# Optimization experiments

Hardware: AMD Instinct MI355X
Metric: run time of the kernel (lower is better)

The kernel has to match this reference:

```python
import jax, jax.numpy as jnp
import numpy as np

KERNEL = 8


def setup_inputs() -> dict:
    key = jax.random.key(0)
    ks = jax.random.split(key, 9)
    N, Cin, L = 16, 128, 2048
    Cout = 256
    x = jax.random.normal(ks[0], (N, Cin, L), dtype=jnp.float32)
    conv_w = jax.random.normal(ks[1], (Cout, Cin, KERNEL), dtype=jnp.float32) * (1.0 / np.sqrt(Cin * KERNEL))
    conv_b = jax.random.normal(ks[2], (Cout,), dtype=jnp.float32) * 0.01
    wq = jax.random.normal(ks[3], (Cout, Cout), dtype=jnp.float32) * (1.0 / np.sqrt(Cout))
    bq = jax.random.normal(ks[4], (Cout,), dtype=jnp.float32) * 0.01
    wk = jax.random.normal(ks[5], (Cout, Cout), dtype=jnp.float32) * (1.0 / np.sqrt(Cout))
    bk = jax.random.normal(ks[6], (Cout,), dtype=jnp.float32) * 0.01
    wv = jax.random.normal(ks[7], (Cout, Cout), dtype=jnp.float32) * (1.0 / np.sqrt(Cout))
    bv = jax.random.normal(ks[8], (Cout,), dtype=jnp.float32) * 0.01
    return {"x": x, "conv_w": conv_w, "conv_b": conv_b,
            "wq": wq, "bq": bq, "wk": wk, "bk": bk, "wv": wv, "bv": bv}


def reference(x, conv_w, conv_b, wq, bq, wk, bk, wv, bv):
    # Conv1d, valid padding: [N, Cin, L] -> [N, Cout, S], S = L - KERNEL + 1
    h = jax.lax.conv_general_dilated(
        x, conv_w, window_strides=(1,), padding='VALID',
        dimension_numbers=('NCH', 'OIH', 'NCH'))
    h = jax.nn.relu(h + conv_b[None, :, None])
    N, C, S = h.shape
    h = jnp.transpose(h, (0, 2, 1))  # [N, S, C]
    # Linear layers (torch convention: y = x @ W^T + b)
    q = jnp.einsum('nsc,dc->nsd', h, wq) + bq
    k = jnp.einsum('nsc,dc->nsd', h, wk) + bk
    v = jnp.einsum('nsc,dc->nsd', h, wv) + bv
    # sigmoid (non-normalized) attention over full SxS scores
    scores = jnp.einsum('nsd,ntd->nst', q, k) / jnp.sqrt(jnp.asarray(C, h.dtype))
    attn = jax.nn.sigmoid(scores)  # [N, S, S]
    out = jnp.einsum('nst,ntd->nsd', attn, v)
    return jnp.transpose(out, (0, 2, 1))  # [N, C, S]
```

## Files before the change

kernel.cpp:

```cpp
#include <hip/hip_runtime.h>

typedef short short8 __attribute__((ext_vector_type(8)));
typedef float f32x4 __attribute__((ext_vector_type(4)));
typedef float f32x16 __attribute__((ext_vector_type(16)));
typedef unsigned short u16x4 __attribute__((ext_vector_type(4)));

constexpr int NB = 16, CIN = 128, LIN = 2048, CO = 256;
constexpr int SL = 2041;
constexpr int MT = NB * SL;
constexpr int MP = 32768;
constexpr int XTS = 136;

constexpr size_t XT_OFF = 0;
constexpr size_t XT_SZ  = (size_t)NB*LIN*XTS*2 + 65536;
constexpr size_t CW_OFF = XT_OFF + XT_SZ;
constexpr size_t CW_SZ  = (size_t)CO*CIN*8*2;
constexpr size_t WQ_OFF = CW_OFF + CW_SZ;
constexpr size_t WB_SZ  = (size_t)CO*CO*2;
constexpr size_t WK_OFF = WQ_OFF + WB_SZ;
constexpr size_t WV_OFF = WK_OFF + WB_SZ;
constexpr size_t H_OFF  = WV_OFF + WB_SZ;
constexpr size_t HB_SZ  = (size_t)MP*CO*2;
constexpr size_t Q_OFF  = H_OFF + HB_SZ;
constexpr size_t K_OFF  = Q_OFF + HB_SZ;
constexpr size_t VT_OFF = K_OFF + HB_SZ;

__device__ inline unsigned short f2bf(float f) {
  union { float f; unsigned int u; } v; v.f = f;
  unsigned int r = v.u + 0x7fffu + ((v.u >> 16) & 1u);
  return (unsigned short)(r >> 16);
}

__device__ inline void sync_lds() {
  __asm__ volatile("" ::: "memory");
  __builtin_amdgcn_s_waitcnt(0xc07f);
  __builtin_amdgcn_s_barrier();
  __asm__ volatile("" ::: "memory");
}
__device__ inline void barrier_only() {
  __asm__ volatile("" ::: "memory");
  __builtin_amdgcn_s_barrier();
  __asm__ volatile("" ::: "memory");
}

#if defined(__has_builtin)
#if __has_builtin(__builtin_amdgcn_global_load_lds)
#define HAVE_GLDS 1
#endif
#endif

__device__ inline void gld16(const unsigned short* g, void* l) {
#ifdef HAVE_GLDS
  __builtin_amdgcn_global_load_lds(
      (const __attribute__((address_space(1))) void*)g,
      (__attribute__((address_space(3))) void*)l, 16, 0, 0);
#else
  *(short8*)l = *(const short8*)g;
#endif
}

__device__ inline unsigned int cvt_pk_bf16(float a, float b) {
  unsigned int r;
  asm("v_cvt_pk_bf16_f32 %0, %1, %2" : "=v"(r) : "v"(a), "v"(b));
  return r;
}
__device__ inline void swap32(unsigned int& a, unsigned int& b) {
  asm("v_permlane32_swap_b32 %0, %1" : "+v"(a), "+v"(b));
}

__global__ void xpose_kernel(const float* __restrict__ x, unsigned short* __restrict__ xt) {
  __shared__ float tile[32][33];
  const int tx = threadIdx.x, ty = threadIdx.y;
  const int s0 = blockIdx.x * 32, c0 = blockIdx.y * 32, n = blockIdx.z;
  #pragma unroll
  for (int r = 0; r < 4; ++r)
    tile[ty * 4 + r][tx] = x[((size_t)(n * CIN + c0 + ty * 4 + r)) * LIN + s0 + tx];
  __syncthreads();
  #pragma unroll
  for (int r = 0; r < 4; ++r)
    xt[((size_t)(n * LIN + s0 + ty * 4 + r)) * XTS + c0 + tx] = f2bf(tile[tx][ty * 4 + r]);
}

__global__ void wconv_kernel(const float* __restrict__ w, unsigned short* __restrict__ o) {
  int idx = blockIdx.x * 256 + threadIdx.x;
  int co = idx >> 10, r = idx & 1023, kp = r >> 7, ci = r & 127;
  o[idx] = f2bf(w[co * 1024 + ci * 8 + kp]);
}

__global__ void wqkv_kernel(const float* __restrict__ a, const float* __restrict__ b,
                            const float* __restrict__ c, unsigned short* __restrict__ oa,
                            unsigned short* __restrict__ ob, unsigned short* __restrict__ oc) {
  int z = blockIdx.x >> 6, lb = blockIdx.x & 63;
  const float* src = (z == 0) ? a : (z == 1) ? b : c;
  unsigned short* dst = (z == 0) ? oa : (z == 1) ? ob : oc;
  int i = (lb * 256 + threadIdx.x) * 4;
  float4 v = *(const float4*)(src + i);
  u16x4 r;
  r.x = f2bf(v.x); r.y = f2bf(v.y); r.z = f2bf(v.z); r.w = f2bf(v.w);
  *(u16x4*)(dst + i) = r;
}

__global__ __launch_bounds__(256) void conv_gemm(
    const unsigned short* __restrict__ xt,
    const unsigned short* __restrict__ wb,
    const float* __restrict__ bias,
    unsigned short* __restrict__ h)
{
  __shared__ unsigned short sX[18432];
  __shared__ unsigned short sB[2][4096];
  const int tid = threadIdx.x;
  const int w = tid >> 6, lane = tid & 63, quad = lane >> 4, l16 = lane & 15;
  const int n  = blockIdx.y;
  const int s0 = blockIdx.x * 128;
  const int d0 = blockIdx.z * 128;

  {
    const unsigned short* xbase = xt + ((size_t)n * LIN + s0) * XTS;
    #pragma unroll
    for (int i = 0; i < 9; ++i) {
      int u = i * 256 + tid;
      gld16(xbase + u * 8, ((char*)sX) + u * 16);
    }
  }

  const int brow0 = tid >> 2, bkgs = tid & 3;
  short8 breg[2];
  #pragma unroll
  for (int i2 = 0; i2 < 2; ++i2) {
    int row = i2 * 64 + brow0;
    int kg = bkgs ^ ((row >> 1) & 3);
    breg[i2] = *(const short8*)(wb + (size_t)(d0 + row) * 1024 + kg * 8);
  }
  #pragma unroll
  for (int i2 = 0; i2 < 2; ++i2)
    *(short8*)(&sB[0][(i2 * 256 + tid) * 8]) = breg[i2];
  __syncthreads();

  f32x4 acc[2][8];
  #pragma unroll
  for (int i = 0; i < 2; ++i)
    #pragma unroll
    for (int j = 0; j < 8; ++j) acc[i][j] = (f32x4){0.f, 0.f, 0.f, 0.f};

  for (int kc = 0; kc < 32; ++kc) {
    const int kcn = (kc < 31) ? kc + 1 : kc;
    const int kpn = kcn >> 2, ci0n = (kcn & 3) * 32;
    #pragma unroll
    for (int i2 = 0; i2 < 2; ++i2) {
      int row = i2 * 64 + brow0;
      int kg = bkgs ^ ((row >> 1) & 3);
      breg[i2] = *(const short8*)(wb + (size_t)(d0 + row) * 1024 + kpn * 128 + ci0n + kg * 8);
    }

    const int kp = kc >> 2, ci0 = (kc & 3) * 32;
    const unsigned short* sBc = sB[kc & 1];
    short8 bfr[8];
    #pragma unroll
    for (int j = 0; j < 8; ++j) {
      int r = j * 16 + l16;
      bfr[j] = *(const short8*)(sBc + r * 32 + (quad ^ ((r >> 1) & 3)) * 8);
    }
    #pragma unroll
    for (int i = 0; i < 2; ++i) {
      int srow = w * 32 + i * 16 + l16;
      short8 afr = *(const short8*)(sX + (srow + kp) * XTS + ci0 + quad * 8);
      #pragma unroll
      for (int j = 0; j < 8; ++j)
        acc[i][j] = __builtin_amdgcn_mfma_f32_16x16x32_bf16(afr, bfr[j], acc[i][j], 0, 0, 0);
    }

    #pragma unroll
    for (int i2 = 0; i2 < 2; ++i2)
      *(short8*)(&sB[(kc + 1) & 1][(i2 * 256 + tid) * 8]) = breg[i2];
    sync_lds();
  }

  #pragma unroll
  for (int i = 0; i < 2; ++i)
    #pragma unroll
    for (int j = 0; j < 8; ++j) {
      int col = d0 + j * 16 + l16;
      float bv = bias[col];
      #pragma unroll
      for (int jj = 0; jj < 4; ++jj) {
        int s = s0 + w * 32 + i * 16 + quad * 4 + jj;
        if (s < SL) {
          float val = fmaxf(acc[i][j][jj] + bv, 0.f);
          h[(size_t)(n * SL + s) * CO + col] = f2bf(val);
        }
      }
    }
}

__global__ __launch_bounds__(256) void lin_gemm(
    const unsigned short* __restrict__ A,
    const unsigned short* __restrict__ Bq, const unsigned short* __restrict__ Bk,
    const unsigned short* __restrict__ Bv,
    const float* __restrict__ biq, const float* __restrict__ bik,
    const float* __restrict__ biv,
    unsigned short* __restrict__ qb, unsigned short* __restrict__ kb,
    unsigned short* __restrict__ vtb)
{
  __shared__ unsigned short sA[2][4096];
  __shared__ unsigned short sB[2][4096];
  const int tid = threadIdx.x;
  const int w = tid >> 6, lane = tid & 63, quad = lane >> 4, l16 = lane & 15;
  const int m0 = blockIdx.x * 128, d0 = blockIdx.y * 128, z = blockIdx.z;
  const unsigned short* B = (z == 0) ? Bq : (z == 1) ? Bk : Bv;
  const float* bias        = (z == 0) ? biq : (z == 1) ? bik : biv;

  const int brow0 = tid >> 2, bkgs = tid & 3;
  short8 areg[2], breg[2];
  #pragma unroll
  for (int i2 = 0; i2 < 2; ++i2) {
    int row = i2 * 64 + brow0;
    int kg = bkgs ^ ((row >> 1) & 3);
    areg[i2] = *(const short8*)(A + (size_t)(m0 + row) * CO + kg * 8);
    breg[i2] = *(const short8*)(B + (size_t)(d0 + row) * CO + kg * 8);
  }
  #pragma unroll
  for (int i2 = 0; i2 < 2; ++i2) {
    *(short8*)(&sA[0][(i2 * 256 + tid) * 8]) = areg[i2];
    *(short8*)(&sB[0][(i2 * 256 + tid) * 8]) = breg[i2];
  }
  sync_lds();

  f32x4 acc[2][8];
  #pragma unroll
  for (int i = 0; i < 2; ++i)
    #pragma unroll
    for (int j = 0; j < 8; ++j) acc[i][j] = (f32x4){0.f, 0.f, 0.f, 0.f};

  for (int kc = 0; kc < 8; ++kc) {
    const int kcn = (kc < 7) ? kc + 1 : kc;
    #pragma unroll
    for (int i2 = 0; i2 < 2; ++i2) {
      int row = i2 * 64 + brow0;
      int kg = bkgs ^ ((row >> 1) & 3);
      areg[i2] = *(const short8*)(A + (size_t)(m0 + row) * CO + kcn * 32 + kg * 8);
      breg[i2] = *(const short8*)(B + (size_t)(d0 + row) * CO + kcn * 32 + kg * 8);
    }

    const unsigned short* sAc = sA[kc & 1];
    const unsigned short* sBc = sB[kc & 1];
    short8 afr[2], bfr[8];
    #pragma unroll
    for (int i = 0; i < 2; ++i) {
      int r = w * 32 + i * 16 + l16;
      afr[i] = *(const short8*)(sAc + r * 32 + (quad ^ ((r >> 1) & 3)) * 8);
    }
    #pragma unroll
    for (int j = 0; j < 8; ++j) {
      int r = j * 16 + l16;
      bfr[j] = *(const short8*)(sBc + r * 32 + (quad ^ ((r >> 1) & 3)) * 8);
    }
    #pragma unroll
    for (int i = 0; i < 2; ++i)
      #pragma unroll
      for (int j = 0; j < 8; ++j)
        acc[i][j] = __builtin_amdgcn_mfma_f32_16x16x32_bf16(afr[i], bfr[j], acc[i][j], 0, 0, 0);

    #pragma unroll
    for (int i2 = 0; i2 < 2; ++i2) {
      *(short8*)(&sA[(kc + 1) & 1][(i2 * 256 + tid) * 8]) = areg[i2];
      *(short8*)(&sB[(kc + 1) & 1][(i2 * 256 + tid) * 8]) = breg[i2];
    }
    sync_lds();
  }

  #pragma unroll
  for (int i = 0; i < 2; ++i)
    #pragma unroll
    for (int j = 0; j < 8; ++j) {
      int col = d0 + j * 16 + l16;
      float bv = bias[col];
      #pragma unroll
      for (int jj = 0; jj < 4; ++jj) {
        int m = m0 + w * 32 + i * 16 + quad * 4 + jj;
        float val = acc[i][j][jj] + bv;
        if (z == 0) {
          qb[(size_t)m * CO + col] = f2bf(val * 0.0625f);
        } else if (z == 1) {
          kb[(size_t)m * CO + col] = f2bf(val);
        } else if (m < MT) {
          int nn = m / SL, ss = m - nn * SL;
          vtb[(size_t)col * MP + nn * 2048 + ss] = f2bf(val);
        }
      }
    }
}

__global__ __launch_bounds__(512, 2) void attn_kernel(
    const unsigned short* __restrict__ qb,
    const unsigned short* __restrict__ kb,
    const unsigned short* __restrict__ vtb,
    float* __restrict__ out)
{
  __shared__ unsigned short sK[2][16384];
  __shared__ unsigned short sV[2][16384];
  const int tid = threadIdx.x;
  const int w = tid >> 6, lane = tid & 63;
  const int half = lane >> 5, l32 = lane & 31;
  const int bidx = blockIdx.x;
  const int n = (bidx & 7) + ((bidx >> 7) << 3);
  const int s0 = ((bidx >> 3) & 15) * 128;
  const int sr = w & 3, tr = w >> 2;

  const unsigned short* kbN = kb + (size_t)(n * SL) * CO;
  const unsigned short* vbN = vtb + (size_t)n * 2048;

#define STAGE_TILE(buf, tk)                                                      \
  {                                                                              \
    _Pragma("unroll")                                                            \
    for (int i = 0; i < 4; ++i) {                                                \
      int u = i * 512 + tid;                                                     \
      int t = u >> 5, sl = u & 31;                                               \
      gld16(kbN + (size_t)((tk) + t) * CO + ((sl ^ (t & 31)) << 3),              \
            ((char*)sK[buf]) + u * 16);                                          \
    }                                                                            \
    _Pragma("unroll")                                                            \
    for (int i = 0; i < 4; ++i) {                                                \
      int u = i * 512 + tid;                                                     \
      int d = u >> 3, sl = u & 7;                                                \
      gld16(vbN + (size_t)d * MP + (tk) + ((sl ^ (d & 7)) << 3),                 \
            ((char*)sV[buf]) + u * 16);                                          \
    }                                                                            \
  }

  STAGE_TILE(0, 0)

  short8 qf[16];
  {
    const unsigned short* qp = qb + (size_t)(n * SL + s0 + sr * 32 + l32) * CO + half * 8;
    #pragma unroll
    for (int kk = 0; kk < 16; ++kk) qf[kk] = *(const short8*)(qp + kk * 16);
  }

  __builtin_amdgcn_s_waitcnt(0x0F70);
  barrier_only();

  f32x16 o[8];
  #pragma unroll
  for (int di = 0; di < 8; ++di)
    #pragma unroll
    for (int r = 0; r < 16; ++r) o[di][r] = 0.f;

  for (int it = 0; it < 32; ++it) {
    const int cur = it & 1;
    if (it < 31) STAGE_TILE(cur ^ 1, (it + 1) * 64)

    const unsigned short* sKc = sK[cur];
    const int tl = tr * 32 + l32;
    f32x16 sacc;
    #pragma unroll
    for (int r = 0; r < 16; ++r) sacc[r] = 0.f;
    __builtin_amdgcn_s_setprio(1);
    #pragma unroll
    for (int kk = 0; kk < 16; ++kk) {
      short8 kf = *(const short8*)(sKc + tl * 256 + (((kk * 2 + half) ^ (tl & 31)) << 3));
      sacc = __builtin_amdgcn_mfma_f32_32x32x16_bf16(kf, qf[kk], sacc, 0, 0, 0);
    }
    __builtin_amdgcn_s_setprio(0);

    #pragma unroll
    for (int r = 0; r < 16; ++r)
      sacc[r] = __builtin_amdgcn_rcpf(1.f + __expf(-sacc[r]));
    if (it == 31 && tr == 1) {
      #pragma unroll
      for (int r = 0; r < 16; ++r) {
        int tloc = (r & 3) + 8 * (r >> 2) + 4 * half;
        if (tloc >= 25) sacc[r] = 0.f;
      }
    }

    short8 pa[2];
    #pragma unroll
    for (int kx = 0; kx < 2; ++kx) {
      unsigned int x0 = cvt_pk_bf16(sacc[kx * 8 + 0], sacc[kx * 8 + 1]);
      unsigned int x1 = cvt_pk_bf16(sacc[kx * 8 + 2], sacc[kx * 8 + 3]);
      unsigned int y0 = cvt_pk_bf16(sacc[kx * 8 + 4], sacc[kx * 8 + 5]);
      unsigned int y1 = cvt_pk_bf16(sacc[kx * 8 + 6], sacc[kx * 8 + 7]);
      swap32(x0, y0);
      swap32(x1, y1);
      union { unsigned int u[4]; short8 s; } pu;
      pu.u[0] = x0; pu.u[1] = x1; pu.u[2] = y0; pu.u[3] = y1;
      pa[kx] = pu.s;
    }

    const unsigned short* sVc = sV[cur];
    __builtin_amdgcn_s_setprio(1);
    #pragma unroll
    for (int kx = 0; kx < 2; ++kx) {
      const int c8 = tr * 4 + kx * 2 + half;
      #pragma unroll
      for (int di = 0; di < 8; ++di) {
        int d = di * 32 + l32;
        short8 vf = *(const short8*)(sVc + d * 64 + ((c8 ^ (d & 7)) << 3));
        o[di] = __builtin_amdgcn_mfma_f32_32x32x16_bf16(vf, pa[kx], o[di], 0, 0, 0);
      }
    }
    __builtin_amdgcn_s_setprio(0);

    if (it < 31) __builtin_amdgcn_s_waitcnt(0x0F70);
    sync_lds();
  }

  {
    unsigned short* myreg = (w < 4) ? (&sK[0][0] + (size_t)w * 8192)
                                    : (&sV[0][0] + (size_t)(w - 4) * 8192);
    const int sb = (tr ^ 1) * 4;
    #pragma unroll
    for (int di = 0; di < 4; ++di)
      #pragma unroll
      for (int q = 0; q < 4; ++q) {
        f32x4 v;
        #pragma unroll
        for (int j = 0; j < 4; ++j) v[j] = o[sb + di][q * 4 + j];
        *(f32x4*)((char*)myreg + (di * 4 + q) * 1024 + lane * 16) = v;
      }
  }
  sync_lds();
  {
    const int pw = w ^ 4;
    const unsigned short* preg = (pw < 4) ? (&sK[0][0] + (size_t)pw * 8192)
                                          : (&sV[0][0] + (size_t)(pw - 4) * 8192);
    const int kb_ = tr * 4;
    const int s = s0 + sr * 32 + l32;
    if (s < SL) {
      float* op = out + (size_t)n * CO * SL + s;
      #pragma unroll
      for (int di = 0; di < 4; ++di)
        #pragma unroll
        for (int q = 0; q < 4; ++q) {
          f32x4 v = *(const f32x4*)((const char*)preg + (di * 4 + q) * 1024 + lane * 16);
          #pragma unroll
          for (int j = 0; j < 4; ++j) {
            int r = q * 4 + j;
            int d = (kb_ + di) * 32 + (r & 3) + 8 * (r >> 2) + 4 * half;
            __builtin_nontemporal_store(o[kb_ + di][r] + v[j], op + (size_t)d * SL);
          }
        }
    }
  }
#undef STAGE_TILE
}

extern "C" void kernel_launch(void* const* d_in, const int* in_sizes, int n_in,
                              void* d_out, int out_size, void* d_ws, size_t ws_size,
                              hipStream_t stream) {
  const float* x      = (const float*)d_in[0];
  const float* conv_w = (const float*)d_in[1];
  const float* conv_b = (const float*)d_in[2];
  const float* wq     = (const float*)d_in[3];
  const float* bq     = (const float*)d_in[4];
  const float* wk     = (const float*)d_in[5];
  const float* bk     = (const float*)d_in[6];
  const float* wv     = (const float*)d_in[7];
  const float* bv     = (const float*)d_in[8];

  char* ws = (char*)d_ws;
  unsigned short* xt  = (unsigned short*)(ws + XT_OFF);
  unsigned short* cw  = (unsigned short*)(ws + CW_OFF);
  unsigned short* wqb = (unsigned short*)(ws + WQ_OFF);
  unsigned short* wkb = (unsigned short*)(ws + WK_OFF);
  unsigned short* wvb = (unsigned short*)(ws + WV_OFF);
  unsigned short* hb  = (unsigned short*)(ws + H_OFF);
  unsigned short* qb  = (unsigned short*)(ws + Q_OFF);
  unsigned short* kb  = (unsigned short*)(ws + K_OFF);
  unsigned short* vtb = (unsigned short*)(ws + VT_OFF);

  hipLaunchKernelGGL(xpose_kernel, dim3(64, 4, 16), dim3(32, 8), 0, stream, x, xt);
  hipLaunchKernelGGL(wconv_kernel, dim3(1024), dim3(256), 0, stream, conv_w, cw);
  hipLaunchKernelGGL(wqkv_kernel,  dim3(192), dim3(256), 0, stream,
                     wq, wk, wv, wqb, wkb, wvb);
  hipLaunchKernelGGL(conv_gemm, dim3(16, 16, 2), dim3(256), 0, stream, xt, cw, conv_b, hb);
  hipLaunchKernelGGL(lin_gemm,  dim3(256, 2, 3), dim3(256), 0, stream,
                     hb, wqb, wkb, wvb, bq, bk, bv, qb, kb, vtb);
  hipLaunchKernelGGL(attn_kernel, dim3(256), dim3(512), 0, stream,
                     qb, kb, vtb, (float*)d_out);
}
```

Before: 261.3 us.

## Drop split-key wave pairs in attention; each wave handles full key tile

Attention blocks shrink from 8 waves to 4. Each wave now iterates over both 32-row halves of every key tile instead of pairing waves across halves, which removes the final LDS reduction of partial outputs and its extra barrier. In exchange, each CU holds fewer waves to hide LDS and MFMA latency, and each thread issues twice as many staging loads.

Result: no change. 259.3 us (-0.8%).

```diff
diff --git a/kernel.cpp b/kernel.cpp
--- a/kernel.cpp
+++ b/kernel.cpp
@@ -290,7 +290,7 @@
     }
 }
 
-__global__ __launch_bounds__(512, 2) void attn_kernel(
+__global__ __launch_bounds__(256, 1) void attn_kernel(
     const unsigned short* __restrict__ qb,
     const unsigned short* __restrict__ kb,
     const unsigned short* __restrict__ vtb,
@@ -304,7 +304,6 @@
   const int bidx = blockIdx.x;
   const int n = (bidx & 7) + ((bidx >> 7) << 3);
   const int s0 = ((bidx >> 3) & 15) * 128;
-  const int sr = w & 3, tr = w >> 2;
 
   const unsigned short* kbN = kb + (size_t)(n * SL) * CO;
   const unsigned short* vbN = vtb + (size_t)n * 2048;
@@ -312,15 +311,15 @@
 #define STAGE_TILE(buf, tk)                                                      \
   {                                                                              \
     _Pragma("unroll")                                                            \
-    for (int i = 0; i < 4; ++i) {                                                \
-      int u = i * 512 + tid;                                                     \
+    for (int i = 0; i < 8; ++i) {                                                \
+      int u = i * 256 + tid;                                                     \
       int t = u >> 5, sl = u & 31;                                               \
       gld16(kbN + (size_t)((tk) + t) * CO + ((sl ^ (t & 31)) << 3),              \
             ((char*)sK[buf]) + u * 16);                                          \
     }                                                                            \
     _Pragma("unroll")                                                            \
-    for (int i = 0; i < 4; ++i) {                                                \
-      int u = i * 512 + tid;                                                     \
+    for (int i = 0; i < 8; ++i) {                                                \
+      int u = i * 256 + tid;                                                     \
       int d = u >> 3, sl = u & 7;                                                \
       gld16(vbN + (size_t)d * MP + (tk) + ((sl ^ (d & 7)) << 3),                 \
             ((char*)sV[buf]) + u * 16);                                          \
@@ -331,7 +330,7 @@
 
   short8 qf[16];
   {
-    const unsigned short* qp = qb + (size_t)(n * SL + s0 + sr * 32 + l32) * CO + half * 8;
+    const unsigned short* qp = qb + (size_t)(n * SL + s0 + w * 32 + l32) * CO + half * 8;
     #pragma unroll
     for (int kk = 0; kk < 16; ++kk) qf[kk] = *(const short8*)(qp + kk * 16);
   }
@@ -350,97 +349,75 @@
     if (it < 31) STAGE_TILE(cur ^ 1, (it + 1) * 64)
 
     const unsigned short* sKc = sK[cur];
-    const int tl = tr * 32 + l32;
-    f32x16 sacc;
-    #pragma unroll
-    for (int r = 0; r < 16; ++r) sacc[r] = 0.f;
-    __builtin_amdgcn_s_setprio(1);
-    #pragma unroll
-    for (int kk = 0; kk < 16; ++kk) {
-      short8 kf = *(const short8*)(sKc + tl * 256 + (((kk * 2 + half) ^ (tl & 31)) << 3));
-      sacc = __builtin_amdgcn_mfma_f32_32x32x16_bf16(kf, qf[kk], sacc, 0, 0, 0);
-    }
-    __builtin_amdgcn_s_setprio(0);
-
-    #pragma unroll
-    for (int r = 0; r < 16; ++r)
-      sacc[r] = __builtin_amdgcn_rcpf(1.f + __expf(-sacc[r]));
-    if (it == 31 && tr == 1) {
-      #pragma unroll
-      for (int r = 0; r < 16; ++r) {
-        int tloc = (r & 3) + 8 * (r >> 2) + 4 * half;
-        if (tloc >= 25) sacc[r] = 0.f;
-      }
-    }
-
-    short8 pa[2];
-    #pragma unroll
-    for (int kx = 0; kx < 2; ++kx) {
-      unsigned int x0 = cvt_pk_bf16(sacc[kx * 8 + 0], sacc[kx * 8 + 1]);
-      unsigned int x1 = cvt_pk_bf16(sacc[kx * 8 + 2], sacc[kx * 8 + 3]);
-      unsigned int y0 = cvt_pk_bf16(sacc[kx * 8 + 4], sacc[kx * 8 + 5]);
-      unsigned int y1 = cvt_pk_bf16(sacc[kx * 8 + 6], sacc[kx * 8 + 7]);
-      swap32(x0, y0);
-      swap32(x1, y1);
-      union { unsigned int u[4]; short8 s; } pu;
-      pu.u[0] = x0; pu.u[1] = x1; pu.u[2] = y0; pu.u[3] = y1;
-      pa[kx] = pu.s;
-    }
-
     const unsigned short* sVc = sV[cur];
-    __builtin_amdgcn_s_setprio(1);
-    #pragma unroll
-    for (int kx = 0; kx < 2; ++kx) {
-      const int c8 = tr * 4 + kx * 2 + half;
-      #pragma unroll
-      for (int di = 0; di < 8; ++di) {
-        int d = di * 32 + l32;
-        short8 vf = *(const short8*)(sVc + d * 64 + ((c8 ^ (d & 7)) << 3));
-        o[di] = __builtin_amdgcn_mfma_f32_32x32x16_bf16(vf, pa[kx], o[di], 0, 0, 0);
-      }
-    }
-    __builtin_amdgcn_s_setprio(0);
+
+    #pragma unroll
+    for (int th = 0; th < 2; ++th) {
+      const int tl = th * 32 + l32;
+      f32x16 sacc;
+      #pragma unroll
+      for (int r = 0; r < 16; ++r) sacc[r] = 0.f;
+      __builtin_amdgcn_s_setprio(1);
+      #pragma unroll
+      for (int kk = 0; kk < 16; ++kk) {
+        short8 kf = *(const short8*)(sKc + tl * 256 + (((kk * 2 + half) ^ (tl & 31)) << 3));
+        sacc = __builtin_amdgcn_mfma_f32_32x32x16_bf16(kf, qf[kk], sacc, 0, 0, 0);
+      }
+      __builtin_amdgcn_s_setprio(0);
+
+      #pragma unroll
+      for (int r = 0; r < 16; ++r)
+        sacc[r] = __builtin_amdgcn_rcpf(1.f + __expf(-sacc[r]));
+      if (it == 31 && th == 1) {
+        #pragma unroll
+        for (int r = 0; r < 16; ++r) {
+          int tloc = (r & 3) + 8 * (r >> 2) + 4 * half;
+          if (tloc >= 25) sacc[r] = 0.f;
+        }
+      }
+
+      short8 pa[2];
+      #pragma unroll
+      for (int kx = 0; kx < 2; ++kx) {
+        unsigned int x0 = cvt_pk_bf16(sacc[kx * 8 + 0], sacc[kx * 8 + 1]);
+        unsigned int x1 = cvt_pk_bf16(sacc[kx * 8 + 2], sacc[kx * 8 + 3]);
+        unsigned int y0 = cvt_pk_bf16(sacc[kx * 8 + 4], sacc[kx * 8 + 5]);
+        unsigned int y1 = cvt_pk_bf16(sacc[kx * 8 + 6], sacc[kx * 8 + 7]);
+        swap32(x0, y0);
+        swap32(x1, y1);
+        union { unsigned int u[4]; short8 s; } pu;
+        pu.u[0] = x0; pu.u[1] = x1; pu.u[2] = y0; pu.u[3] = y1;
+        pa[kx] = pu.s;
+      }
+
+      __builtin_amdgcn_s_setprio(1);
+      #pragma unroll
+      for (int kx = 0; kx < 2; ++kx) {
+        const int c8 = th * 4 + kx * 2 + half;
+        #pragma unroll
+        for (int di = 0; di < 8; ++di) {
+          int d = di * 32 + l32;
+          short8 vf = *(const short8*)(sVc + d * 64 + ((c8 ^ (d & 7)) << 3));
+          o[di] = __builtin_amdgcn_mfma_f32_32x32x16_bf16(vf, pa[kx], o[di], 0, 0, 0);
+        }
+      }
+      __builtin_amdgcn_s_setprio(0);
+    }
 
     if (it < 31) __builtin_amdgcn_s_waitcnt(0x0F70);
     sync_lds();
   }
 
-  {
-    unsigned short* myreg = (w < 4) ? (&sK[0][0] + (size_t)w * 8192)
-                                    : (&sV[0][0] + (size_t)(w - 4) * 8192);
-    const int sb = (tr ^ 1) * 4;
-    #pragma unroll
-    for (int di = 0; di < 4; ++di)
-      #pragma unroll
-      for (int q = 0; q < 4; ++q) {
-        f32x4 v;
-        #pragma unroll
-        for (int j = 0; j < 4; ++j) v[j] = o[sb + di][q * 4 + j];
-        *(f32x4*)((char*)myreg + (di * 4 + q) * 1024 + lane * 16) = v;
-      }
-  }
-  sync_lds();
-  {
-    const int pw = w ^ 4;
-    const unsigned short* preg = (pw < 4) ? (&sK[0][0] + (size_t)pw * 8192)
-                                          : (&sV[0][0] + (size_t)(pw - 4) * 8192);
-    const int kb_ = tr * 4;
-    const int s = s0 + sr * 32 + l32;
-    if (s < SL) {
-      float* op = out + (size_t)n * CO * SL + s;
-      #pragma unroll
-      for (int di = 0; di < 4; ++di)
-        #pragma unroll
-        for (int q = 0; q < 4; ++q) {
-          f32x4 v = *(const f32x4*)((const char*)preg + (di * 4 + q) * 1024 + lane * 16);
-          #pragma unroll
-          for (int j = 0; j < 4; ++j) {
-            int r = q * 4 + j;
-            int d = (kb_ + di) * 32 + (r & 3) + 8 * (r >> 2) + 4 * half;
-            __builtin_nontemporal_store(o[kb_ + di][r] + v[j], op + (size_t)d * SL);
-          }
-        }
-    }
+  const int s = s0 + w * 32 + l32;
+  if (s < SL) {
+    float* op = out + (size_t)n * CO * SL + s;
+    #pragma unroll
+    for (int di = 0; di < 8; ++di)
+      #pragma unroll
+      for (int r = 0; r < 16; ++r) {
+        int d = di * 32 + (r & 3) + 8 * (r >> 2) + 4 * half;
+        __builtin_nontemporal_store(o[di][r], op + (size_t)d * SL);
+      }
   }
 #undef STAGE_TILE
 }
@@ -476,6 +453,6 @@
   hipLaunchKernelGGL(conv_gemm, dim3(16, 16, 2), dim3(256), 0, stream, xt, cw, conv_b, hb);
   hipLaunchKernelGGL(lin_gemm,  dim3(256, 2, 3), dim3(256), 0, stream,
                      hb, wqb, wkb, wvb, bq, bk, bv, qb, kb, vtb);
-  hipLaunchKernelGGL(attn_kernel, dim3(256), dim3(512), 0, stream,
+  hipLaunchKernelGGL(attn_kernel, dim3(256), dim3(256), 0, stream,
                      qb, kb, vtb, (float*)d_out);
 }
```
